# Performance work log

Measured on AMD Instinct MI355X. Metric: run time of the kernel, lower is better.

Reference implementation:

```python
import jax, jax.numpy as jnp
import numpy as np

B, L, D_MODEL = 2, 1024, 1024
D_STATE, D_CONV, EXPAND, HEADDIM = 64, 4, 2, 64
D_INNER = EXPAND * D_MODEL              # 2048
NHEADS = D_INNER // HEADDIM             # 32
NGROUPS = 1
CONV_DIM = D_INNER + 2 * NGROUPS * D_STATE            # 2176
D_IN_PROJ = 2 * D_INNER + 2 * NGROUPS * D_STATE + NHEADS  # 4256
RMS_EPS = 1e-6      # block nn.RMSNorm eps
GATED_EPS = 1e-5    # Mamba2 RMSNormGated eps

def _rmsnorm(x, w, eps):
    return x * jax.lax.rsqrt(jnp.mean(x * x, axis=-1, keepdims=True) + eps) * w

def _silu(x):
    return x * jax.nn.sigmoid(x)

def _mamba2(x, W_in, conv_w, conv_b, dt_bias, A_log, D_param, ssm_norm_w, W_out):
    b, l, _ = x.shape
    zxbcdt = x @ W_in.T                                   # (b,l,D_IN_PROJ)
    z = zxbcdt[..., :D_INNER]
    xBC = zxbcdt[..., D_INNER:D_INNER + CONV_DIM]
    dt = zxbcdt[..., D_INNER + CONV_DIM:]                 # (b,l,H)
    # depthwise causal conv1d (kernel D_CONV) + silu
    pad = jnp.pad(xBC, ((0, 0), (D_CONV - 1, 0), (0, 0)))
    conv = conv_b + sum(pad[:, i:i + l, :] * conv_w[:, i] for i in range(D_CONV))
    xBC = _silu(conv)
    xs = xBC[..., :D_INNER].reshape(b, l, NHEADS, HEADDIM)
    Bm = xBC[..., D_INNER:D_INNER + D_STATE]              # (b,l,N), ngroups=1
    Cm = xBC[..., D_INNER + D_STATE:]                     # (b,l,N)
    dt = jax.nn.softplus(dt + dt_bias)                    # (b,l,H)
    dA = jnp.exp(dt * (-jnp.exp(A_log)))                  # (b,l,H)
    dtx = dt[..., None] * xs                              # (b,l,H,P)

    def step(h, inp):
        dA_t, dtx_t, B_t, C_t = inp
        h = h * dA_t[:, :, None, None] + dtx_t[..., None] * B_t[:, None, None, :]
        y_t = jnp.einsum('bhpn,bn->bhp', h, C_t)
        return h, y_t

    h0 = jnp.zeros((b, NHEADS, HEADDIM, D_STATE), x.dtype)
    _, ys = jax.lax.scan(step, h0, (dA.transpose(1, 0, 2), dtx.transpose(1, 0, 2, 3),
                                    Bm.transpose(1, 0, 2), Cm.transpose(1, 0, 2)))
    y = ys.transpose(1, 0, 2, 3) + xs * D_param[None, None, :, None]
    y = y.reshape(b, l, D_INNER)
    y = _rmsnorm(y * _silu(z), ssm_norm_w, GATED_EPS)     # RMSNormGated, norm_before_gate=False
    return y @ W_out.T

def _block(x, x_d, norm_w, W_in, conv_w, conv_b, dt_bias, A_log, D_param, ssm_norm_w, W_out, w1, w2):
    # dual_residual=True, residual_scale=1.0, dropout is identity (eval)
    x_ln = _rmsnorm(x, norm_w, RMS_EPS)
    x_f = _mamba2(x_ln, W_in, conv_w, conv_b, dt_bias, A_log, D_param, ssm_norm_w, W_out)
    x_a = x + x_f
    x_f_scaled = x_f
    x_ln = _rmsnorm(x_a, norm_w, RMS_EPS)
    g = x_ln @ w1.T
    x_f = (g * jax.nn.sigmoid(g)) * (x_ln @ w2.T)         # SwiGLU
    x_a = x_a + x_f
    x_f_scaled = x_f_scaled + x_f
    return x_a, x_d + x_f_scaled

def setup_inputs() -> dict:
    key = jax.random.key(0)
    ks = jax.random.split(key, 12)
    dt = jax.random.uniform(ks[6], (NHEADS,), minval=1e-3, maxval=0.1)
    return {
        'x': jax.random.normal(ks[0], (B, L, D_MODEL), jnp.float32),
        'x_d': jax.random.normal(ks[1], (B, L, D_MODEL), jnp.float32),
        'norm_w': jnp.ones((D_MODEL,), jnp.float32),
        'W_in': jax.random.normal(ks[2], (D_IN_PROJ, D_MODEL), jnp.float32) * (D_MODEL ** -0.5),
        'conv_w': jax.random.normal(ks[3], (CONV_DIM, D_CONV), jnp.float32) * 0.2,
        'conv_b': jnp.zeros((CONV_DIM,), jnp.float32),
        'dt_bias': dt + jnp.log(-jnp.expm1(-dt)),   # inverse softplus of dt
        'A_log': jnp.log(jax.random.uniform(ks[7], (NHEADS,), minval=1.0, maxval=16.0)),
        'D_param': jnp.ones((NHEADS,), jnp.float32),
        'ssm_norm_w': jnp.ones((D_INNER,), jnp.float32),
        'W_out': jax.random.normal(ks[4], (D_MODEL, D_INNER), jnp.float32) * (D_INNER ** -0.5),
        'w1': jax.random.normal(ks[8], (D_MODEL, D_MODEL), jnp.float32) * (D_MODEL ** -0.5),
        'w2': jax.random.normal(ks[9], (D_MODEL, D_MODEL), jnp.float32) * (D_MODEL ** -0.5),
    }

def reference(x, x_d, norm_w, W_in, conv_w, conv_b, dt_bias, A_log, D_param, ssm_norm_w, W_out, w1, w2):
    return _block(x, x_d, norm_w, W_in, conv_w, conv_b, dt_bias, A_log, D_param, ssm_norm_w, W_out, w1, w2)
```

## Files before the change

kernel.cpp:

```cpp
#include <hip/hip_runtime.h>

typedef unsigned short u16;
typedef __attribute__((ext_vector_type(8))) short bf16x8;
typedef __attribute__((ext_vector_type(4))) float f32x4;

#define B_      2
#define L_      1024
#define DM      1024
#define DI      2048
#define NH      32
#define HD      64
#define DSTATE  64
#define CONVD   2176
#define DPROJ   4256
#define ZXS     4352

__device__ __forceinline__ u16 f2bf(float f) {
  union { float f; unsigned u; } v; v.f = f;
  unsigned r = v.u + 0x7fffu + ((v.u >> 16) & 1u);
  return (u16)(r >> 16);
}

__device__ __forceinline__ void load_lds16(const void* g, void* l) {
  __builtin_amdgcn_global_load_lds(
      (const __attribute__((address_space(1))) void*)g,
      (__attribute__((address_space(3))) void*)l, 16, 0, 0);
}

__device__ __forceinline__ float block_reduce_sum256(float v) {
  #pragma unroll
  for (int off = 32; off > 0; off >>= 1) v += __shfl_down(v, off, 64);
  __shared__ float red[4];
  int lane = threadIdx.x & 63, w = threadIdx.x >> 6;
  if (lane == 0) red[w] = v;
  __syncthreads();
  return red[0] + red[1] + red[2] + red[3];
}

__global__ __launch_bounds__(256) void convert_weights(
    const float* __restrict__ W_in, const float* __restrict__ W_out,
    const float* __restrict__ w1, const float* __restrict__ w2,
    u16* __restrict__ Winb, u16* __restrict__ Woutb, u16* __restrict__ w12b) {
  const long R0 = 4256L * 1024 / 4;
  const long R1 = R0 + 2048L * 1024 / 4;
  long i = (long)blockIdx.x * 256 + threadIdx.x;
  float4 v;
  ushort4* dst;
  if (i < R0) {
    v = ((const float4*)W_in)[i];
    dst = ((ushort4*)Winb) + i;
  } else if (i < R1) {
    long j = i - R0;
    v = ((const float4*)W_out)[j];
    dst = ((ushort4*)Woutb) + j;
  } else {
    long j = i - R1;
    long row = j >> 8;
    long col = j & 255;
    const float* s = (row & 1) ? w2 : w1;
    v = ((const float4*)s)[(row >> 1) * 256 + col];
    dst = ((ushort4*)w12b) + j;
  }
  *dst = make_ushort4(f2bf(v.x), f2bf(v.y), f2bf(v.z), f2bf(v.w));
}

__global__ __launch_bounds__(256) void add_rms_kernel(
    const float* __restrict__ in1, const float* __restrict__ in2,
    float* __restrict__ sum_out, const float* __restrict__ wt,
    u16* __restrict__ out, float eps) {
  const int row = blockIdx.x;
  const int c = threadIdx.x << 2;
  float4 v = *(const float4*)(in1 + (long)row * DM + c);
  if (in2) {
    float4 u = *(const float4*)(in2 + (long)row * DM + c);
    v.x += u.x; v.y += u.y; v.z += u.z; v.w += u.w;
  }
  if (sum_out) *(float4*)(sum_out + (long)row * DM + c) = v;
  float ss = v.x * v.x + v.y * v.y + v.z * v.z + v.w * v.w;
  float tot = block_reduce_sum256(ss);
  float sc = rsqrtf(tot * (1.0f / DM) + eps);
  float4 wv = *(const float4*)(wt + c);
  *(ushort4*)(out + (long)row * DM + c) =
      make_ushort4(f2bf(v.x * sc * wv.x), f2bf(v.y * sc * wv.y),
                   f2bf(v.z * sc * wv.z), f2bf(v.w * sc * wv.w));
}

template<int NJ>
__global__ __launch_bounds__(256) void gemm_lds(
    const u16* __restrict__ A, const u16* __restrict__ Bw,
    float* __restrict__ C, int N, int Nw, int K) {
  constexpr int BN = NJ * 32;
  __shared__ u16 As[2][128][64];
  __shared__ u16 Bs[2][BN][64];
  const int tid = threadIdx.x;
  const int lane = tid & 63;
  const int wave = tid >> 6;
  const int ml = lane & 15;
  const int quad = lane >> 4;
  const int wm = (wave & 1) << 6;
  const int wn = (wave >> 1) * (BN / 2);
  const long bm = (long)blockIdx.y << 7;
  const long bn = (long)blockIdx.x * BN;

  const int lr = lane >> 3;
  const int lc = (lane & 7) ^ lr;

  f32x4 acc[4][NJ];
  #pragma unroll
  for (int i = 0; i < 4; ++i)
    #pragma unroll
    for (int j = 0; j < NJ; ++j)
      acc[i][j] = (f32x4){0.f, 0.f, 0.f, 0.f};

  auto stage = [&](int kk, int buf) {
    #pragma unroll
    for (int t = 0; t < 4; ++t) {
      const int u = wave * 4 + t;
      const u16* g = A + (bm + u * 8 + lr) * K + kk + lc * 8;
      load_lds16(g, &As[buf][u * 8][0]);
    }
    #pragma unroll
    for (int t = 0; t < NJ; ++t) {
      const int u = wave * NJ + t;
      long brow = bn + u * 8 + lr;
      if (brow >= Nw) brow = Nw - 1;
      const u16* g = Bw + brow * K + kk + lc * 8;
      load_lds16(g, &Bs[buf][u * 8][0]);
    }
  };

  stage(0, 0);
  int buf = 0;
  for (int kt = 0; kt < K; kt += 64) {
    if (kt + 64 < K) {
      stage(kt + 64, buf ^ 1);
      if constexpr (NJ == 4)
        asm volatile("s_waitcnt vmcnt(8)\n\ts_barrier" ::: "memory");
      else
        asm volatile("s_waitcnt vmcnt(6)\n\ts_barrier" ::: "memory");
    } else {
      asm volatile("s_waitcnt vmcnt(0)\n\ts_barrier" ::: "memory");
    }
    #pragma unroll
    for (int ks = 0; ks < 2; ++ks) {
      const int c = ks * 4 + quad;
      const int pc = (c ^ (ml & 7)) << 3;
      bf16x8 af[4], bfr[NJ];
      #pragma unroll
      for (int i = 0; i < 4; ++i)
        af[i] = *(const bf16x8*)&As[buf][wm + (i << 4) + ml][pc];
      #pragma unroll
      for (int j = 0; j < NJ; ++j)
        bfr[j] = *(const bf16x8*)&Bs[buf][wn + (j << 4) + ml][pc];
      #pragma unroll
      for (int i = 0; i < 4; ++i)
        #pragma unroll
        for (int j = 0; j < NJ; ++j)
          acc[i][j] = __builtin_amdgcn_mfma_f32_16x16x32_bf16(af[i], bfr[j], acc[i][j], 0, 0, 0);
    }
    asm volatile("s_barrier" ::: "memory");
    buf ^= 1;
  }

  const int rquad = quad << 2;
  #pragma unroll
  for (int i = 0; i < 4; ++i) {
    const long gm = bm + wm + (i << 4) + rquad;
    #pragma unroll
    for (int j = 0; j < NJ; ++j) {
      const long gn = bn + wn + (j << 4) + ml;
      #pragma unroll
      for (int r = 0; r < 4; ++r)
        C[(gm + r) * N + gn] = acc[i][j][r];
    }
  }
}

__global__ __launch_bounds__(256) void gemm_mlp_final(
    const u16* __restrict__ A, const u16* __restrict__ Bw,
    const float* __restrict__ xa, const float* __restrict__ xd,
    const float* __restrict__ xf, float* __restrict__ out, int K) {
  constexpr int NJ = 4;
  constexpr int BN = 128;
  __shared__ u16 As[2][128][64];
  __shared__ u16 Bs[2][BN][64];
  const int tid = threadIdx.x;
  const int lane = tid & 63;
  const int wave = tid >> 6;
  const int ml = lane & 15;
  const int quad = lane >> 4;
  const int wm = (wave & 1) << 6;
  const int wn = (wave >> 1) * 64;
  const long bm = (long)blockIdx.y << 7;
  const long bn = (long)blockIdx.x * BN;

  const int lr = lane >> 3;
  const int lc = (lane & 7) ^ lr;

  f32x4 acc[4][NJ];
  #pragma unroll
  for (int i = 0; i < 4; ++i)
    #pragma unroll
    for (int j = 0; j < NJ; ++j)
      acc[i][j] = (f32x4){0.f, 0.f, 0.f, 0.f};

  auto stage = [&](int kk, int buf) {
    #pragma unroll
    for (int t = 0; t < 4; ++t) {
      const int u = wave * 4 + t;
      load_lds16(A + (bm + u * 8 + lr) * K + kk + lc * 8, &As[buf][u * 8][0]);
    }
    #pragma unroll
    for (int t = 0; t < NJ; ++t) {
      const int u = wave * NJ + t;
      load_lds16(Bw + (bn + u * 8 + lr) * K + kk + lc * 8, &Bs[buf][u * 8][0]);
    }
  };

  stage(0, 0);
  int buf = 0;
  for (int kt = 0; kt < K; kt += 64) {
    if (kt + 64 < K) {
      stage(kt + 64, buf ^ 1);
      asm volatile("s_waitcnt vmcnt(8)\n\ts_barrier" ::: "memory");
    } else {
      asm volatile("s_waitcnt vmcnt(0)\n\ts_barrier" ::: "memory");
    }
    #pragma unroll
    for (int ks = 0; ks < 2; ++ks) {
      const int c = ks * 4 + quad;
      const int pc = (c ^ (ml & 7)) << 3;
      bf16x8 af[4], bfr[NJ];
      #pragma unroll
      for (int i = 0; i < 4; ++i)
        af[i] = *(const bf16x8*)&As[buf][wm + (i << 4) + ml][pc];
      #pragma unroll
      for (int j = 0; j < NJ; ++j)
        bfr[j] = *(const bf16x8*)&Bs[buf][wn + (j << 4) + ml][pc];
      #pragma unroll
      for (int i = 0; i < 4; ++i)
        #pragma unroll
        for (int j = 0; j < NJ; ++j)
          acc[i][j] = __builtin_amdgcn_mfma_f32_16x16x32_bf16(af[i], bfr[j], acc[i][j], 0, 0, 0);
    }
    asm volatile("s_barrier" ::: "memory");
    buf ^= 1;
  }

  float* out1 = out + (long)B_ * L_ * DM;
  const int rquad = quad << 2;
  #pragma unroll
  for (int i = 0; i < 4; ++i) {
    const long gm = bm + wm + (i << 4) + rquad;
    #pragma unroll
    for (int j = 0; j < NJ; ++j) {
      const long gn = bn + wn + (j << 4) + ml;
      #pragma unroll
      for (int r = 0; r < 4; ++r) {
        float v = acc[i][j][r];
        float p = __shfl_xor(v, 1, 64);
        if ((ml & 1) == 0) {
          float e = (v / (1.f + expf(-v))) * p;
          long row = gm + r;
          long col = gn >> 1;
          long o = row * DM + col;
          out[o]  = xa[o] + e;
          out1[o] = xd[o] + xf[o] + e;
        }
      }
    }
  }
}

__global__ __launch_bounds__(256) void conv_silu_kernel(
    const float* __restrict__ zx, const float* __restrict__ cw,
    const float* __restrict__ cb, float* __restrict__ xc) {
  int idx = blockIdx.x * 256 + threadIdx.x;
  if (idx >= 2048 * 544) return;
  const int c4 = (idx % 544) << 2;
  const int row = idx / 544;
  const int t = row & (L_ - 1);
  float4 acc = *(const float4*)(cb + c4);
  float4 w0 = *(const float4*)(cw + (c4 + 0) * 4);
  float4 w1v = *(const float4*)(cw + (c4 + 1) * 4);
  float4 w2v = *(const float4*)(cw + (c4 + 2) * 4);
  float4 w3v = *(const float4*)(cw + (c4 + 3) * 4);
  const float wts[4][4] = {{w0.x, w0.y, w0.z, w0.w},
                           {w1v.x, w1v.y, w1v.z, w1v.w},
                           {w2v.x, w2v.y, w2v.z, w2v.w},
                           {w3v.x, w3v.y, w3v.z, w3v.w}};
  #pragma unroll
  for (int i = 0; i < 4; ++i) {
    int tau = t - 3 + i;
    if (tau >= 0) {
      float4 xv = *(const float4*)(zx + (long)(row - t + tau) * ZXS + DI + c4);
      acc.x = fmaf(xv.x, wts[0][i], acc.x);
      acc.y = fmaf(xv.y, wts[1][i], acc.y);
      acc.z = fmaf(xv.z, wts[2][i], acc.z);
      acc.w = fmaf(xv.w, wts[3][i], acc.w);
    }
  }
  acc.x = acc.x / (1.f + expf(-acc.x));
  acc.y = acc.y / (1.f + expf(-acc.y));
  acc.z = acc.z / (1.f + expf(-acc.z));
  acc.w = acc.w / (1.f + expf(-acc.w));
  *(float4*)(xc + (long)row * CONVD + c4) = acc;
}

__global__ __launch_bounds__(256) void ssd_chunk_kernel(
    const float* __restrict__ xc, const float* __restrict__ zx,
    const float* __restrict__ dt_bias, const float* __restrict__ A_log,
    float* __restrict__ yss, float* __restrict__ Sbuf,
    float* __restrict__ EGbuf, float* __restrict__ Lam) {
  const int c = blockIdx.x & 15;
  const int h = (blockIdx.x >> 4) & 31;
  const int b = blockIdx.x >> 9;
  const int bh = b * NH + h;
  const long crow = (long)b * L_ + c * 64;
  const int tid = threadIdx.x, lane = tid & 63, wave = tid >> 6;

  __shared__ u16 Cs[64][72], Bs[64][72], Xt[64][72], Btw[64][72], Ms[64][72];
  __shared__ float Gs[64], wjL[64], dtL[64];

  if (wave == 0) {
    float draw = zx[(crow + lane) * ZXS + (DI + CONVD) + h] + dt_bias[h];
    float dt = (draw > 20.f) ? draw : log1pf(expf(draw));
    float g = -expf(A_log[h]) * dt;
    float G = g;
    #pragma unroll
    for (int off = 1; off < 64; off <<= 1) {
      float t = __shfl_up(G, off, 64);
      if (lane >= off) G += t;
    }
    float G63 = __shfl(G, 63, 64);
    Gs[lane] = G;
    wjL[lane] = expf(G63 - G) * dt;
    dtL[lane] = dt;
    EGbuf[(bh * 16 + c) * 64 + lane] = expf(G);
    if (lane == 63) Lam[bh * 16 + c] = expf(G63);
  }
  __syncthreads();
  for (int idx = tid; idx < 1024; idx += 256) {
    int r = idx >> 4, c4 = (idx & 15) << 2;
    const float* row = xc + (crow + r) * CONVD;
    float4 xv = *(const float4*)(row + h * HD + c4);
    Xt[c4 + 0][r] = f2bf(xv.x); Xt[c4 + 1][r] = f2bf(xv.y);
    Xt[c4 + 2][r] = f2bf(xv.z); Xt[c4 + 3][r] = f2bf(xv.w);
    float4 bv = *(const float4*)(row + DI + c4);
    *(ushort4*)&Bs[r][c4] = make_ushort4(f2bf(bv.x), f2bf(bv.y), f2bf(bv.z), f2bf(bv.w));
    float w = wjL[r];
    Btw[c4 + 0][r] = f2bf(bv.x * w); Btw[c4 + 1][r] = f2bf(bv.y * w);
    Btw[c4 + 2][r] = f2bf(bv.z * w); Btw[c4 + 3][r] = f2bf(bv.w * w);
    float4 cv = *(const float4*)(row + DI + DSTATE + c4);
    *(ushort4*)&Cs[r][c4] = make_ushort4(f2bf(cv.x), f2bf(cv.y), f2bf(cv.z), f2bf(cv.w));
  }
  __syncthreads();

  const int mrow = wave * 16 + (lane & 15);
  const int quad = lane >> 4;
  f32x4 accE[4];
  #pragma unroll
  for (int j = 0; j < 4; ++j) accE[j] = (f32x4){0.f, 0.f, 0.f, 0.f};
  #pragma unroll
  for (int ks = 0; ks < 2; ++ks) {
    int k0 = ks * 32 + quad * 8;
    bf16x8 a = *(const bf16x8*)&Cs[mrow][k0];
    #pragma unroll
    for (int j = 0; j < 4; ++j) {
      bf16x8 bfr = *(const bf16x8*)&Bs[j * 16 + (lane & 15)][k0];
      accE[j] = __builtin_amdgcn_mfma_f32_16x16x32_bf16(a, bfr, accE[j], 0, 0, 0);
    }
  }
  #pragma unroll
  for (int j = 0; j < 4; ++j) {
    int jc = j * 16 + (lane & 15);
    float Gj = Gs[jc], dtj = dtL[jc];
    #pragma unroll
    for (int r = 0; r < 4; ++r) {
      int ir = wave * 16 + quad * 4 + r;
      float v = (ir >= jc) ? accE[j][r] * expf(Gs[ir] - Gj) * dtj : 0.f;
      Ms[ir][jc] = f2bf(v);
    }
  }
  __syncthreads();
  f32x4 accY[4], accS[4];
  #pragma unroll
  for (int j = 0; j < 4; ++j) { accY[j] = (f32x4){0.f,0.f,0.f,0.f}; accS[j] = (f32x4){0.f,0.f,0.f,0.f}; }
  #pragma unroll
  for (int ks = 0; ks < 2; ++ks) {
    int k0 = ks * 32 + quad * 8;
    bf16x8 aM = *(const bf16x8*)&Ms[mrow][k0];
    bf16x8 aX = *(const bf16x8*)&Xt[mrow][k0];
    #pragma unroll
    for (int j = 0; j < 4; ++j) {
      bf16x8 bX = *(const bf16x8*)&Xt[j * 16 + (lane & 15)][k0];
      bf16x8 bB = *(const bf16x8*)&Btw[j * 16 + (lane & 15)][k0];
      accY[j] = __builtin_amdgcn_mfma_f32_16x16x32_bf16(aM, bX, accY[j], 0, 0, 0);
      accS[j] = __builtin_amdgcn_mfma_f32_16x16x32_bf16(aX, bB, accS[j], 0, 0, 0);
    }
  }
  float* Sc = Sbuf + (long)(bh * 16 + c) * 4096;
  #pragma unroll
  for (int j = 0; j < 4; ++j) {
    int col = j * 16 + (lane & 15);
    #pragma unroll
    for (int r = 0; r < 4; ++r) {
      int mr = wave * 16 + quad * 4 + r;
      yss[(crow + mr) * DI + h * HD + col] = accY[j][r];
      Sc[mr * 64 + col] = accS[j][r];
    }
  }
}

__global__ __launch_bounds__(256) void ssd_combine_kernel(
    float* __restrict__ Sbuf, const float* __restrict__ Lam) {
  const int bh = blockIdx.x >> 4;
  const int e = (blockIdx.x & 15) * 256 + threadIdx.x;
  float* base = Sbuf + (long)bh * 16 * 4096 + e;
  const float* lamp = Lam + bh * 16;
  float H = 0.f;
  for (int cc = 0; cc < 16; ++cc) {
    float lam = lamp[cc];
    float v = base[cc * 4096];
    base[cc * 4096] = H;
    H = fmaf(lam, H, v);
  }
}

__global__ __launch_bounds__(256) void ssd_final_kernel(
    const float* __restrict__ xc, const float* __restrict__ Sbuf,
    const float* __restrict__ EGbuf, const float* __restrict__ Dp,
    float* __restrict__ yss) {
  const int c = blockIdx.x & 15;
  const int h = (blockIdx.x >> 4) & 31;
  const int b = blockIdx.x >> 9;
  const int bh = b * NH + h;
  const long crow = (long)b * L_ + c * 64;
  const int tid = threadIdx.x, lane = tid & 63, wave = tid >> 6;
  __shared__ u16 Csc[64][72], Hs[64][72];
  __shared__ float egL[64];
  if (tid < 64) egL[tid] = EGbuf[(bh * 16 + c) * 64 + tid];
  __syncthreads();
  const float* Sc = Sbuf + (long)(bh * 16 + c) * 4096;
  for (int idx = tid; idx < 1024; idx += 256) {
    int r = idx >> 4, c4 = (idx & 15) << 2;
    float4 hv = *(const float4*)(Sc + r * 64 + c4);
    *(ushort4*)&Hs[r][c4] = make_ushort4(f2bf(hv.x), f2bf(hv.y), f2bf(hv.z), f2bf(hv.w));
    float eg = egL[r];
    float4 cv = *(const float4*)(xc + (crow + r) * CONVD + DI + DSTATE + c4);
    *(ushort4*)&Csc[r][c4] = make_ushort4(f2bf(cv.x * eg), f2bf(cv.y * eg),
                                          f2bf(cv.z * eg), f2bf(cv.w * eg));
  }
  __syncthreads();
  const int mrow = wave * 16 + (lane & 15);
  const int quad = lane >> 4;
  f32x4 acc[4];
  #pragma unroll
  for (int j = 0; j < 4; ++j) acc[j] = (f32x4){0.f, 0.f, 0.f, 0.f};
  #pragma unroll
  for (int ks = 0; ks < 2; ++ks) {
    int k0 = ks * 32 + quad * 8;
    bf16x8 a = *(const bf16x8*)&Csc[mrow][k0];
    #pragma unroll
    for (int j = 0; j < 4; ++j) {
      bf16x8 bfr = *(const bf16x8*)&Hs[j * 16 + (lane & 15)][k0];
      acc[j] = __builtin_amdgcn_mfma_f32_16x16x32_bf16(a, bfr, acc[j], 0, 0, 0);
    }
  }
  const float Dh = Dp[h];
  #pragma unroll
  for (int j = 0; j < 4; ++j) {
    int p = j * 16 + (lane & 15);
    #pragma unroll
    for (int r = 0; r < 4; ++r) {
      int ir = wave * 16 + quad * 4 + r;
      long o = (crow + ir) * DI + h * HD + p;
      float xval = xc[(crow + ir) * CONVD + h * HD + p];
      yss[o] = yss[o] + acc[j][r] + Dh * xval;
    }
  }
}

__global__ __launch_bounds__(256) void gated_rms_kernel(
    const float* __restrict__ y, const float* __restrict__ zx,
    const float* __restrict__ wt, u16* __restrict__ out) {
  const int row = blockIdx.x;
  const int c = threadIdx.x << 3;
  const float* yr = y + (long)row * DI + c;
  const float* zr = zx + (long)row * ZXS + c;
  float v[8];
  float ss = 0.f;
  #pragma unroll
  for (int i = 0; i < 8; i += 4) {
    float4 y4 = *(const float4*)(yr + i);
    float4 z4 = *(const float4*)(zr + i);
    const float zz[4] = {z4.x, z4.y, z4.z, z4.w};
    const float yy[4] = {y4.x, y4.y, y4.z, y4.w};
    #pragma unroll
    for (int j = 0; j < 4; ++j) {
      float sg = zz[j] / (1.f + expf(-zz[j]));
      float val = yy[j] * sg;
      v[i + j] = val;
      ss += val * val;
    }
  }
  float tot = block_reduce_sum256(ss);
  float sc = rsqrtf(tot * (1.0f / DI) + 1e-5f);
  const float* wr = wt + c;
  *(ushort4*)(out + (long)row * DI + c) =
      make_ushort4(f2bf(v[0] * sc * wr[0]), f2bf(v[1] * sc * wr[1]),
                   f2bf(v[2] * sc * wr[2]), f2bf(v[3] * sc * wr[3]));
  *(ushort4*)(out + (long)row * DI + c + 4) =
      make_ushort4(f2bf(v[4] * sc * wr[4]), f2bf(v[5] * sc * wr[5]),
                   f2bf(v[6] * sc * wr[6]), f2bf(v[7] * sc * wr[7]));
}

extern "C" void kernel_launch(void* const* d_in, const int* in_sizes, int n_in,
                              void* d_out, int out_size, void* d_ws, size_t ws_size,
                              hipStream_t stream) {
  const float* x        = (const float*)d_in[0];
  const float* x_d      = (const float*)d_in[1];
  const float* norm_w   = (const float*)d_in[2];
  const float* W_in     = (const float*)d_in[3];
  const float* conv_w   = (const float*)d_in[4];
  const float* conv_b   = (const float*)d_in[5];
  const float* dt_bias  = (const float*)d_in[6];
  const float* A_log    = (const float*)d_in[7];
  const float* D_param  = (const float*)d_in[8];
  const float* ssm_w    = (const float*)d_in[9];
  const float* W_out    = (const float*)d_in[10];
  const float* w1       = (const float*)d_in[11];
  const float* w2       = (const float*)d_in[12];
  float* out = (float*)d_out;

  char* wsc = (char*)d_ws;
  size_t off = 0;
  auto alloc = [&](size_t n) { char* p = wsc + off; off += (n + 255) & ~(size_t)255; return p; };
  float* zx   = (float*)alloc((size_t)2048 * ZXS * 4);
  float* xc   = (float*)alloc((size_t)2048 * 2176 * 4);
  float* yss  = (float*)alloc((size_t)2048 * 2048 * 4);
  float* xf   = (float*)alloc((size_t)2048 * 1024 * 4);
  float* xa   = (float*)alloc((size_t)2048 * 1024 * 4);
  float* Sbuf = (float*)alloc((size_t)1024 * 16 * 4096 / 16 * 4);
  float* EGbuf= (float*)alloc((size_t)65536 * 4);
  float* Lam  = (float*)alloc((size_t)1024 * 4);
  u16* xlnb   = (u16*)alloc((size_t)2048 * 1024 * 2);
  u16* ygnb   = (u16*)alloc((size_t)2048 * 2048 * 2);
  u16* xln2b  = (u16*)alloc((size_t)2048 * 1024 * 2);
  u16* Winb   = (u16*)alloc((size_t)4256 * 1024 * 2);
  u16* Woutb  = (u16*)alloc((size_t)1024 * 2048 * 2);
  u16* w12b   = (u16*)alloc((size_t)2048 * 1024 * 2);

  convert_weights<<<8352, 256, 0, stream>>>(W_in, W_out, w1, w2, Winb, Woutb, w12b);
  add_rms_kernel<<<2048, 256, 0, stream>>>(x, nullptr, nullptr, norm_w, xlnb, 1e-6f);
  gemm_lds<4><<<dim3(34, 16), 256, 0, stream>>>(xlnb, Winb, zx, ZXS, 4256, 1024);
  conv_silu_kernel<<<(2048 * 544 + 255) / 256, 256, 0, stream>>>(zx, conv_w, conv_b, xc);
  ssd_chunk_kernel<<<1024, 256, 0, stream>>>(xc, zx, dt_bias, A_log, yss, Sbuf, EGbuf, Lam);
  ssd_combine_kernel<<<1024, 256, 0, stream>>>(Sbuf, Lam);
  ssd_final_kernel<<<1024, 256, 0, stream>>>(xc, Sbuf, EGbuf, D_param, yss);
  gated_rms_kernel<<<2048, 256, 0, stream>>>(yss, zx, ssm_w, ygnb);
  gemm_lds<2><<<dim3(16, 16), 256, 0, stream>>>(ygnb, Woutb, xf, 1024, 1024, 2048);
  add_rms_kernel<<<2048, 256, 0, stream>>>(x, xf, xa, norm_w, xln2b, 1e-6f);
  gemm_mlp_final<<<dim3(16, 16), 256, 0, stream>>>(xln2b, w12b, xa, x_d, xf, out, 1024);
}
```

Measured before the change: 288.3 us.

## Shrink GEMM tiles for more blocks and de-interleave MLP gate/up weights

Makes the GEMM M-tile a template parameter and uses smaller tiles (64x128 for in-proj, 64x64 for out-proj, 64-row tiles for the MLP), which roughly doubles the number of workgroups. The aim is to fill the GPU's compute units better. The MLP weight layout changes from row-interleaved w1/w2 to stacked blocks. Each tile then loads matching gate and up rows and applies the SiLU product in registers, with no cross-lane shuffle and no half-idle lanes. Smaller tiles lower data reuse per block and add more global traffic.

```diff
diff --git a/kernel.cpp b/kernel.cpp
--- a/kernel.cpp
+++ b/kernel.cpp
@@ -25,6 +25,12 @@
   __builtin_amdgcn_global_load_lds(
       (const __attribute__((address_space(1))) void*)g,
       (__attribute__((address_space(3))) void*)l, 16, 0, 0);
+}
+
+template<int P> __device__ __forceinline__ void wait_prefetch() {
+  if constexpr (P == 4)      asm volatile("s_waitcnt vmcnt(4)\n\ts_barrier" ::: "memory");
+  else if constexpr (P == 6) asm volatile("s_waitcnt vmcnt(6)\n\ts_barrier" ::: "memory");
+  else if constexpr (P == 8) asm volatile("s_waitcnt vmcnt(8)\n\ts_barrier" ::: "memory");
 }
 
 __device__ __forceinline__ float block_reduce_sum256(float v) {
@@ -56,9 +62,8 @@
   } else {
     long j = i - R1;
     long row = j >> 8;
-    long col = j & 255;
-    const float* s = (row & 1) ? w2 : w1;
-    v = ((const float4*)s)[(row >> 1) * 256 + col];
+    const float* s = (row < 1024) ? (w1 + row * 1024) : (w2 + (row - 1024) * 1024);
+    v = ((const float4*)s)[j & 255];
     dst = ((ushort4*)w12b) + j;
   }
   *dst = make_ushort4(f2bf(v.x), f2bf(v.y), f2bf(v.z), f2bf(v.w));
@@ -85,47 +90,46 @@
                    f2bf(v.z * sc * wv.z), f2bf(v.w * sc * wv.w));
 }
 
-template<int NJ>
+template<int NI, int NJ>
 __global__ __launch_bounds__(256) void gemm_lds(
     const u16* __restrict__ A, const u16* __restrict__ Bw,
     float* __restrict__ C, int N, int Nw, int K) {
+  constexpr int BM = NI * 32;
   constexpr int BN = NJ * 32;
-  __shared__ u16 As[2][128][64];
+  __shared__ u16 As[2][BM][64];
   __shared__ u16 Bs[2][BN][64];
   const int tid = threadIdx.x;
   const int lane = tid & 63;
   const int wave = tid >> 6;
   const int ml = lane & 15;
   const int quad = lane >> 4;
-  const int wm = (wave & 1) << 6;
-  const int wn = (wave >> 1) * (BN / 2);
-  const long bm = (long)blockIdx.y << 7;
+  const int wm = (wave & 1) * (NI * 16);
+  const int wn = (wave >> 1) * (NJ * 16);
+  const long bm = (long)blockIdx.y * BM;
   const long bn = (long)blockIdx.x * BN;
 
   const int lr = lane >> 3;
   const int lc = (lane & 7) ^ lr;
 
-  f32x4 acc[4][NJ];
-  #pragma unroll
-  for (int i = 0; i < 4; ++i)
+  f32x4 acc[NI][NJ];
+  #pragma unroll
+  for (int i = 0; i < NI; ++i)
     #pragma unroll
     for (int j = 0; j < NJ; ++j)
       acc[i][j] = (f32x4){0.f, 0.f, 0.f, 0.f};
 
   auto stage = [&](int kk, int buf) {
     #pragma unroll
-    for (int t = 0; t < 4; ++t) {
-      const int u = wave * 4 + t;
-      const u16* g = A + (bm + u * 8 + lr) * K + kk + lc * 8;
-      load_lds16(g, &As[buf][u * 8][0]);
-    }
-    #pragma unroll
-    for (int t = 0; t < NJ; ++t) {
-      const int u = wave * NJ + t;
+    for (int t = 0; t < BM / 32; ++t) {
+      const int u = wave * (BM / 32) + t;
+      load_lds16(A + (bm + u * 8 + lr) * K + kk + lc * 8, &As[buf][u * 8][0]);
+    }
+    #pragma unroll
+    for (int t = 0; t < BN / 32; ++t) {
+      const int u = wave * (BN / 32) + t;
       long brow = bn + u * 8 + lr;
       if (brow >= Nw) brow = Nw - 1;
-      const u16* g = Bw + brow * K + kk + lc * 8;
-      load_lds16(g, &Bs[buf][u * 8][0]);
+      load_lds16(Bw + brow * K + kk + lc * 8, &Bs[buf][u * 8][0]);
     }
   };
 
@@ -134,10 +138,7 @@
   for (int kt = 0; kt < K; kt += 64) {
     if (kt + 64 < K) {
       stage(kt + 64, buf ^ 1);
-      if constexpr (NJ == 4)
-        asm volatile("s_waitcnt vmcnt(8)\n\ts_barrier" ::: "memory");
-      else
-        asm volatile("s_waitcnt vmcnt(6)\n\ts_barrier" ::: "memory");
+      wait_prefetch<NI + NJ>();
     } else {
       asm volatile("s_waitcnt vmcnt(0)\n\ts_barrier" ::: "memory");
     }
@@ -145,15 +146,15 @@
     for (int ks = 0; ks < 2; ++ks) {
       const int c = ks * 4 + quad;
       const int pc = (c ^ (ml & 7)) << 3;
-      bf16x8 af[4], bfr[NJ];
-      #pragma unroll
-      for (int i = 0; i < 4; ++i)
+      bf16x8 af[NI], bfr[NJ];
+      #pragma unroll
+      for (int i = 0; i < NI; ++i)
         af[i] = *(const bf16x8*)&As[buf][wm + (i << 4) + ml][pc];
       #pragma unroll
       for (int j = 0; j < NJ; ++j)
         bfr[j] = *(const bf16x8*)&Bs[buf][wn + (j << 4) + ml][pc];
       #pragma unroll
-      for (int i = 0; i < 4; ++i)
+      for (int i = 0; i < NI; ++i)
         #pragma unroll
         for (int j = 0; j < NJ; ++j)
           acc[i][j] = __builtin_amdgcn_mfma_f32_16x16x32_bf16(af[i], bfr[j], acc[i][j], 0, 0, 0);
@@ -164,7 +165,7 @@
 
   const int rquad = quad << 2;
   #pragma unroll
-  for (int i = 0; i < 4; ++i) {
+  for (int i = 0; i < NI; ++i) {
     const long gm = bm + wm + (i << 4) + rquad;
     #pragma unroll
     for (int j = 0; j < NJ; ++j) {
@@ -180,40 +181,40 @@
     const u16* __restrict__ A, const u16* __restrict__ Bw,
     const float* __restrict__ xa, const float* __restrict__ xd,
     const float* __restrict__ xf, float* __restrict__ out, int K) {
-  constexpr int NJ = 4;
-  constexpr int BN = 128;
-  __shared__ u16 As[2][128][64];
-  __shared__ u16 Bs[2][BN][64];
+  __shared__ u16 As[2][64][64];
+  __shared__ u16 Bs[2][128][64];
   const int tid = threadIdx.x;
   const int lane = tid & 63;
   const int wave = tid >> 6;
   const int ml = lane & 15;
   const int quad = lane >> 4;
-  const int wm = (wave & 1) << 6;
-  const int wn = (wave >> 1) * 64;
-  const long bm = (long)blockIdx.y << 7;
-  const long bn = (long)blockIdx.x * BN;
+  const int wm = (wave & 1) * 32;
+  const int wn = (wave >> 1) * 32;
+  const long bm = (long)blockIdx.y * 64;
+  const long c0 = (long)blockIdx.x * 64;
 
   const int lr = lane >> 3;
   const int lc = (lane & 7) ^ lr;
 
-  f32x4 acc[4][NJ];
-  #pragma unroll
-  for (int i = 0; i < 4; ++i)
-    #pragma unroll
-    for (int j = 0; j < NJ; ++j)
+  f32x4 acc[2][4];
+  #pragma unroll
+  for (int i = 0; i < 2; ++i)
+    #pragma unroll
+    for (int j = 0; j < 4; ++j)
       acc[i][j] = (f32x4){0.f, 0.f, 0.f, 0.f};
 
   auto stage = [&](int kk, int buf) {
+    #pragma unroll
+    for (int t = 0; t < 2; ++t) {
+      const int u = wave * 2 + t;
+      load_lds16(A + (bm + u * 8 + lr) * K + kk + lc * 8, &As[buf][u * 8][0]);
+    }
     #pragma unroll
     for (int t = 0; t < 4; ++t) {
       const int u = wave * 4 + t;
-      load_lds16(A + (bm + u * 8 + lr) * K + kk + lc * 8, &As[buf][u * 8][0]);
-    }
-    #pragma unroll
-    for (int t = 0; t < NJ; ++t) {
-      const int u = wave * NJ + t;
-      load_lds16(Bw + (bn + u * 8 + lr) * K + kk + lc * 8, &Bs[buf][u * 8][0]);
+      const int r = u * 8 + lr;
+      const long grow = (r < 64) ? (c0 + r) : (1024 + c0 + (r - 64));
+      load_lds16(Bw + grow * K + kk + lc * 8, &Bs[buf][u * 8][0]);
     }
   };
 
@@ -222,7 +223,7 @@
   for (int kt = 0; kt < K; kt += 64) {
     if (kt + 64 < K) {
       stage(kt + 64, buf ^ 1);
-      asm volatile("s_waitcnt vmcnt(8)\n\ts_barrier" ::: "memory");
+      wait_prefetch<6>();
     } else {
       asm volatile("s_waitcnt vmcnt(0)\n\ts_barrier" ::: "memory");
     }
@@ -230,17 +231,19 @@
     for (int ks = 0; ks < 2; ++ks) {
       const int c = ks * 4 + quad;
       const int pc = (c ^ (ml & 7)) << 3;
-      bf16x8 af[4], bfr[NJ];
-      #pragma unroll
-      for (int i = 0; i < 4; ++i)
+      bf16x8 af[2], bfr[4];
+      #pragma unroll
+      for (int i = 0; i < 2; ++i)
         af[i] = *(const bf16x8*)&As[buf][wm + (i << 4) + ml][pc];
       #pragma unroll
-      for (int j = 0; j < NJ; ++j)
-        bfr[j] = *(const bf16x8*)&Bs[buf][wn + (j << 4) + ml][pc];
-      #pragma unroll
-      for (int i = 0; i < 4; ++i)
+      for (int j = 0; j < 2; ++j) {
+        bfr[j]     = *(const bf16x8*)&Bs[buf][wn + (j << 4) + ml][pc];
+        bfr[j + 2] = *(const bf16x8*)&Bs[buf][64 + wn + (j << 4) + ml][pc];
+      }
+      #pragma unroll
+      for (int i = 0; i < 2; ++i)
         #pragma unroll
-        for (int j = 0; j < NJ; ++j)
+        for (int j = 0; j < 4; ++j)
           acc[i][j] = __builtin_amdgcn_mfma_f32_16x16x32_bf16(af[i], bfr[j], acc[i][j], 0, 0, 0);
     }
     asm volatile("s_barrier" ::: "memory");
@@ -250,23 +253,19 @@
   float* out1 = out + (long)B_ * L_ * DM;
   const int rquad = quad << 2;
   #pragma unroll
-  for (int i = 0; i < 4; ++i) {
+  for (int i = 0; i < 2; ++i) {
     const long gm = bm + wm + (i << 4) + rquad;
     #pragma unroll
-    for (int j = 0; j < NJ; ++j) {
-      const long gn = bn + wn + (j << 4) + ml;
+    for (int jj = 0; jj < 2; ++jj) {
+      const long col = c0 + wn + (jj << 4) + ml;
       #pragma unroll
       for (int r = 0; r < 4; ++r) {
-        float v = acc[i][j][r];
-        float p = __shfl_xor(v, 1, 64);
-        if ((ml & 1) == 0) {
-          float e = (v / (1.f + expf(-v))) * p;
-          long row = gm + r;
-          long col = gn >> 1;
-          long o = row * DM + col;
-          out[o]  = xa[o] + e;
-          out1[o] = xd[o] + xf[o] + e;
-        }
+        float g = acc[i][jj][r];
+        float h = acc[i][jj + 2][r];
+        float e = (g / (1.f + expf(-g))) * h;
+        long o = (gm + r) * DM + col;
+        out[o]  = xa[o] + e;
+        out1[o] = xd[o] + xf[o] + e;
       }
     }
   }
@@ -541,7 +540,7 @@
   float* yss  = (float*)alloc((size_t)2048 * 2048 * 4);
   float* xf   = (float*)alloc((size_t)2048 * 1024 * 4);
   float* xa   = (float*)alloc((size_t)2048 * 1024 * 4);
-  float* Sbuf = (float*)alloc((size_t)1024 * 16 * 4096 / 16 * 4);
+  float* Sbuf = (float*)alloc((size_t)64 * 16 * 4096 * 4);
   float* EGbuf= (float*)alloc((size_t)65536 * 4);
   float* Lam  = (float*)alloc((size_t)1024 * 4);
   u16* xlnb   = (u16*)alloc((size_t)2048 * 1024 * 2);
@@ -553,13 +552,13 @@
 
   convert_weights<<<8352, 256, 0, stream>>>(W_in, W_out, w1, w2, Winb, Woutb, w12b);
   add_rms_kernel<<<2048, 256, 0, stream>>>(x, nullptr, nullptr, norm_w, xlnb, 1e-6f);
-  gemm_lds<4><<<dim3(34, 16), 256, 0, stream>>>(xlnb, Winb, zx, ZXS, 4256, 1024);
+  gemm_lds<4, 2><<<dim3(68, 16), 256, 0, stream>>>(xlnb, Winb, zx, ZXS, 4256, 1024);
   conv_silu_kernel<<<(2048 * 544 + 255) / 256, 256, 0, stream>>>(zx, conv_w, conv_b, xc);
   ssd_chunk_kernel<<<1024, 256, 0, stream>>>(xc, zx, dt_bias, A_log, yss, Sbuf, EGbuf, Lam);
   ssd_combine_kernel<<<1024, 256, 0, stream>>>(Sbuf, Lam);
   ssd_final_kernel<<<1024, 256, 0, stream>>>(xc, Sbuf, EGbuf, D_param, yss);
   gated_rms_kernel<<<2048, 256, 0, stream>>>(yss, zx, ssm_w, ygnb);
-  gemm_lds<2><<<dim3(16, 16), 256, 0, stream>>>(ygnb, Woutb, xf, 1024, 1024, 2048);
+  gemm_lds<2, 2><<<dim3(16, 32), 256, 0, stream>>>(ygnb, Woutb, xf, 1024, 1024, 2048);
   add_rms_kernel<<<2048, 256, 0, stream>>>(x, xf, xa, norm_w, xln2b, 1e-6f);
-  gemm_mlp_final<<<dim3(16, 16), 256, 0, stream>>>(xln2b, w12b, xa, x_d, xf, out, 1024);
-}
+  gemm_mlp_final<<<dim3(16, 32), 256, 0, stream>>>(xln2b, w12b, xa, x_d, xf, out, 1024);
+}
```

After: 261.5 us. -9.3%, faster.
